# Optimization experiments

Hardware: AMD Instinct MI355X
Metric: run time of the kernel (lower is better)

Reference implementation:

```python
import jax, jax.numpy as jnp
import numpy as np
import math

COEFF_SHIFT_ARRAY = [0, 63, 31, 21, 15, 12, 10, 9, 7, 7, 6, 5, 5, 4, 4, 4, 3, 3, 3, 3, 3, 3, 2, 2, 2, 2, 2, 2, 2, 2, 2, 2, 1, 1, 1, 1, 1, 1, 1, 1, 1, 1, 1, 1, 1, 1, 1, 1, 1, 1, 1, 1, 1, 1, 1, 1, 1, 1, 1, 1, 1, 1, 1, 1]

MAX_VAL = 1023.0          # (1 << 10) - 1
QSTEP = 25.5
DEAD_ZONE_OFFSET = 85.0 / 512.0


def make_orthonormal_dct2_matrix(n):
    x = np.arange(n, dtype=np.float64).reshape(1, n)
    k = np.arange(n, dtype=np.float64).reshape(n, 1)
    mat = np.cos(math.pi / n * (x + 0.5) * k)
    mat[0, :] *= math.sqrt(1.0 / n)
    mat[1:, :] *= math.sqrt(2.0 / n)
    return jnp.asarray(mat, dtype=jnp.float32)


def setup_inputs() -> dict:
    key = jax.random.key(0)
    residual_norm = jax.random.normal(key, (256, 64, 32, 32), dtype=jnp.float32) * 0.1
    dct_mat = make_orthonormal_dct2_matrix(32)           # [32, 32], Ch == Cw
    coeff_shift = jnp.asarray(COEFF_SHIFT_ARRAY, dtype=jnp.float32)  # [64]
    return {"residual_norm": residual_norm, "dct_mat": dct_mat, "coeff_shift": coeff_shift}


def reference(residual_norm, dct_mat, coeff_shift):
    C = dct_mat
    # scale to integer-like domain
    x = residual_norm * MAX_VAL                                   # [B,Ch,H,W]
    # DCT2: coeff = C @ x @ C.T
    tmp = jnp.einsum('kh,bchw->bckw', C, x)
    coeff = jnp.einsum('lw,bckw->bckl', C, tmp)
    # dead-zone quantize with STE
    sgn = jnp.sign(coeff)
    q_abs_real = jnp.abs(coeff) / QSTEP + DEAD_ZONE_OFFSET
    q_hat = jnp.floor(q_abs_real) * sgn
    q_real = q_abs_real * sgn
    qcoeff = q_real + jax.lax.stop_gradient(q_hat - q_real)      # STE
    # dequantize with qAbs<64 interpolation correction + STE
    q_abs = jnp.abs(qcoeff)
    q_sgn = jnp.where(qcoeff < 0.0, -1.0, 1.0)
    coeff_abs = q_abs * QSTEP
    idx = jnp.clip(jax.lax.stop_gradient(q_abs).astype(jnp.int32), 0, 63)
    cs = coeff_shift[idx]
    coeff_abs2 = (q_abs + 1.0) * QSTEP
    coeff_abs_corr = ((1024.0 - cs) * coeff_abs + cs * coeff_abs2) / 1024.0
    coeff_abs_hat = jnp.where(q_abs < 64.0, coeff_abs_corr, coeff_abs)
    coeff_hat_det = coeff_abs_hat * q_sgn
    coeff_real = coeff_abs * q_sgn
    coeff_hat = coeff_real + jax.lax.stop_gradient(coeff_hat_det - coeff_real)  # STE
    # IDCT2: x = C.T @ coeff @ C
    tmp2 = jnp.einsum('hk,bckw->bchw', C, coeff_hat)
    rec = jnp.einsum('wl,bchw->bchl', C, tmp2)
    return rec / MAX_VAL
```

## Files before the change

kernel.cpp:

```cpp
#include <hip/hip_runtime.h>

typedef float f32x4 __attribute__((ext_vector_type(4)));
typedef short s16x8 __attribute__((ext_vector_type(8)));

#define QSTEP 25.5f
#define DZ (85.0f/512.0f)

__device__ __forceinline__ unsigned rne_bf16(float x) {
  unsigned u = __float_as_uint(x);
  return (u + 0x7FFFu + ((u >> 16) & 1u)) >> 16;
}

__global__ __launch_bounds__(256, 4) void vvc_mfma2_kernel(
    const float* __restrict__ resid,
    const float* __restrict__ dct,
    const float* __restrict__ cshift,
    float* __restrict__ out)
{
  __shared__ float shm[64 + 4 * 1152];
  float* Dq   = shm;
  float* Pall = shm + 64;

  const int tid  = threadIdx.x;
  const int wave = tid >> 6;
  const int lane = tid & 63;
  const int col  = lane & 15;
  const int quad = lane >> 4;
  const int k0   = quad * 8;

  unsigned short* Chi  = (unsigned short*)Pall;
  unsigned short* Clo  = Chi + 1280;
  unsigned short* CThi = Chi + 2560;
  {
    float4 cv = ((const float4*)dct)[tid];
    int k = tid >> 3, h = (tid & 7) * 4;
    float vals[4] = {cv.x, cv.y, cv.z, cv.w};
#pragma unroll
    for (int i = 0; i < 4; ++i) {
      unsigned hi = rne_bf16(vals[i]);
      float r = vals[i] - __uint_as_float(hi << 16);
      unsigned lo = rne_bf16(r);
      Chi[k * 40 + h + i]        = (unsigned short)hi;
      Clo[k * 40 + h + i]        = (unsigned short)lo;
      CThi[(h + i) * 40 + k]     = (unsigned short)hi;
    }
    if (tid < 64)
      Dq[tid] = QSTEP * ((float)tid + cshift[tid] * (1.0f / 1024.0f));
  }
  __syncthreads();

  s16x8 aChi[2], aClo[2], bCThi[2];
#pragma unroll
  for (int i = 0; i < 2; ++i) {
    aChi[i]  = *(const s16x8*)(Chi  + (16 * i + col) * 40 + k0);
    aClo[i]  = *(const s16x8*)(Clo  + (16 * i + col) * 40 + k0);
    bCThi[i] = *(const s16x8*)(CThi + (16 * i + col) * 40 + k0);
  }
  __syncthreads();

  float* Pw = Pall + wave * 1152;
  const int tile = blockIdx.x * 4 + wave;
  const float* gx = resid + (size_t)tile * 1024;
  float* gout     = out   + (size_t)tile * 1024;

  s16x8 bXhi[2], bXlo[2];
#pragma unroll
  for (int nj = 0; nj < 2; ++nj) {
#pragma unroll
    for (int j = 0; j < 8; ++j) {
      float x = gx[(k0 + j) * 32 + nj * 16 + col] * 1023.0f;
      unsigned u  = __float_as_uint(x);
      float r = x - __uint_as_float(u & 0xFFFF0000u);
      bXhi[nj][j] = (short)(u >> 16);
      bXlo[nj][j] = (short)(__float_as_uint(r) >> 16);
    }
  }

  f32x4 acc[2][2];

#pragma unroll
  for (int mi = 0; mi < 2; ++mi)
#pragma unroll
    for (int nj = 0; nj < 2; ++nj) acc[mi][nj] = (f32x4)0.0f;
#pragma unroll
  for (int mi = 0; mi < 2; ++mi)
#pragma unroll
    for (int nj = 0; nj < 2; ++nj) {
      acc[mi][nj] = __builtin_amdgcn_mfma_f32_16x16x32_bf16(aChi[mi], bXhi[nj], acc[mi][nj], 0, 0, 0);
      acc[mi][nj] = __builtin_amdgcn_mfma_f32_16x16x32_bf16(aClo[mi], bXhi[nj], acc[mi][nj], 0, 0, 0);
      acc[mi][nj] = __builtin_amdgcn_mfma_f32_16x16x32_bf16(aChi[mi], bXlo[nj], acc[mi][nj], 0, 0, 0);
    }

  unsigned* T = (unsigned*)Pw;
#pragma unroll
  for (int mi = 0; mi < 2; ++mi)
#pragma unroll
    for (int nj = 0; nj < 2; ++nj)
#pragma unroll
      for (int r = 0; r < 4; ++r) {
        float v = acc[mi][nj][r];
        unsigned u = __float_as_uint(v);
        float rr = v - __uint_as_float(u & 0xFFFF0000u);
        T[(16 * mi + 4 * quad + r) * 36 + 16 * nj + col] =
            (u >> 16) | (__float_as_uint(rr) & 0xFFFF0000u);
      }

  s16x8 tHi[2], tLo[2];
#pragma unroll
  for (int mi = 0; mi < 2; ++mi) {
    const unsigned* row = T + (16 * mi + col) * 36 + k0;
    uint4 u0 = *(const uint4*)row, u1 = *(const uint4*)(row + 4);
    s16x8 h, l;
    h[0]=(short)u0.x; h[1]=(short)u0.y; h[2]=(short)u0.z; h[3]=(short)u0.w;
    h[4]=(short)u1.x; h[5]=(short)u1.y; h[6]=(short)u1.z; h[7]=(short)u1.w;
    l[0]=(short)(u0.x>>16); l[1]=(short)(u0.y>>16); l[2]=(short)(u0.z>>16); l[3]=(short)(u0.w>>16);
    l[4]=(short)(u1.x>>16); l[5]=(short)(u1.y>>16); l[6]=(short)(u1.z>>16); l[7]=(short)(u1.w>>16);
    tHi[mi] = h; tLo[mi] = l;
  }
#pragma unroll
  for (int mi = 0; mi < 2; ++mi)
#pragma unroll
    for (int nj = 0; nj < 2; ++nj) acc[mi][nj] = (f32x4)0.0f;
#pragma unroll
  for (int mi = 0; mi < 2; ++mi)
#pragma unroll
    for (int nj = 0; nj < 2; ++nj) {
      acc[mi][nj] = __builtin_amdgcn_mfma_f32_16x16x32_bf16(tHi[mi], aChi[nj], acc[mi][nj], 0, 0, 0);
      acc[mi][nj] = __builtin_amdgcn_mfma_f32_16x16x32_bf16(tLo[mi], aChi[nj], acc[mi][nj], 0, 0, 0);
      acc[mi][nj] = __builtin_amdgcn_mfma_f32_16x16x32_bf16(tHi[mi], aClo[nj], acc[mi][nj], 0, 0, 0);
    }

  unsigned short* WT = (unsigned short*)Pw;
#pragma unroll
  for (int mi = 0; mi < 2; ++mi)
#pragma unroll
    for (int nj = 0; nj < 2; ++nj) {
      unsigned w16[4];
#pragma unroll
      for (int r = 0; r < 4; ++r) {
        float cc  = acc[mi][nj][r];
        float qa  = floorf(fabsf(cc) * (1.0f / QSTEP) + DZ);
        int   qi  = (int)qa; qi = qi > 63 ? 63 : qi;
        float lut = Dq[qi];
        float cah = (qa < 64.0f) ? lut : qa * QSTEP;
        float wv  = (cc < 0.0f) ? -cah : cah;
        w16[r] = rne_bf16(wv);
      }
      uint2 pk; pk.x = w16[0] | (w16[1] << 16); pk.y = w16[2] | (w16[3] << 16);
      *(uint2*)(WT + (16 * nj + col) * 40 + 16 * mi + 4 * quad) = pk;
    }

  s16x8 wA[2];
#pragma unroll
  for (int mi = 0; mi < 2; ++mi)
    wA[mi] = *(const s16x8*)(WT + (16 * mi + col) * 40 + k0);
#pragma unroll
  for (int mi = 0; mi < 2; ++mi)
#pragma unroll
    for (int nj = 0; nj < 2; ++nj) acc[mi][nj] = (f32x4)0.0f;
#pragma unroll
  for (int mi = 0; mi < 2; ++mi)
#pragma unroll
    for (int nj = 0; nj < 2; ++nj)
      acc[mi][nj] = __builtin_amdgcn_mfma_f32_16x16x32_bf16(wA[mi], aChi[nj], acc[mi][nj], 0, 0, 0);

  unsigned short* U = WT;
#pragma unroll
  for (int mi = 0; mi < 2; ++mi)
#pragma unroll
    for (int nj = 0; nj < 2; ++nj) {
      unsigned u16v[4];
#pragma unroll
      for (int r = 0; r < 4; ++r) u16v[r] = rne_bf16(acc[mi][nj][r]);
      uint2 pk; pk.x = u16v[0] | (u16v[1] << 16); pk.y = u16v[2] | (u16v[3] << 16);
      *(uint2*)(U + (16 * nj + col) * 40 + 16 * mi + 4 * quad) = pk;
    }

  s16x8 uA[2];
#pragma unroll
  for (int mi = 0; mi < 2; ++mi)
    uA[mi] = *(const s16x8*)(U + (16 * mi + col) * 40 + k0);
#pragma unroll
  for (int mi = 0; mi < 2; ++mi)
#pragma unroll
    for (int nj = 0; nj < 2; ++nj) acc[mi][nj] = (f32x4)0.0f;
#pragma unroll
  for (int mi = 0; mi < 2; ++mi)
#pragma unroll
    for (int nj = 0; nj < 2; ++nj)
      acc[mi][nj] = __builtin_amdgcn_mfma_f32_16x16x32_bf16(uA[mi], bCThi[nj], acc[mi][nj], 0, 0, 0);

#pragma unroll
  for (int mi = 0; mi < 2; ++mi)
#pragma unroll
    for (int nj = 0; nj < 2; ++nj)
#pragma unroll
      for (int r = 0; r < 4; ++r)
        gout[(16 * mi + 4 * quad + r) * 32 + 16 * nj + col] =
            acc[mi][nj][r] * (1.0f / 1023.0f);
}

extern "C" void kernel_launch(void* const* d_in, const int* in_sizes, int n_in,
                              void* d_out, int out_size, void* d_ws, size_t ws_size,
                              hipStream_t stream) {
  const float* resid  = (const float*)d_in[0];
  const float* dct    = (const float*)d_in[1];
  const float* cshift = (const float*)d_in[2];
  float* out = (float*)d_out;

  int tiles  = out_size / 1024;
  int blocks = tiles / 4;
  vvc_mfma2_kernel<<<blocks, 256, 0, stream>>>(resid, dct, cshift, out);
}
```

Before: 116.6 us.

## Use persistent blocks looping over tiles with register prefetch of next tile

The kernel now launches a fixed grid of 1024 blocks. Each wave loops over several 32x32 tiles, strided by 4096 tiles, and prefetches the next tile's input into registers while it computes the current one. This amortizes the per-block DCT matrix setup and bf16 splitting, and overlaps global loads with the MFMA work. The risks are higher register pressure, fewer resident waves to hide latency, and the assumption that the tile count is a multiple of 4096.

```diff
diff --git a/kernel.cpp b/kernel.cpp
--- a/kernel.cpp
+++ b/kernel.cpp
@@ -15,7 +15,8 @@
     const float* __restrict__ resid,
     const float* __restrict__ dct,
     const float* __restrict__ cshift,
-    float* __restrict__ out)
+    float* __restrict__ out,
+    int niter)
 {
   __shared__ float shm[64 + 4 * 1152];
   float* Dq   = shm;
@@ -59,145 +60,171 @@
   __syncthreads();
 
   float* Pw = Pall + wave * 1152;
-  const int tile = blockIdx.x * 4 + wave;
-  const float* gx = resid + (size_t)tile * 1024;
-  float* gout     = out   + (size_t)tile * 1024;
-
-  s16x8 bXhi[2], bXlo[2];
-#pragma unroll
-  for (int nj = 0; nj < 2; ++nj) {
-#pragma unroll
-    for (int j = 0; j < 8; ++j) {
-      float x = gx[(k0 + j) * 32 + nj * 16 + col] * 1023.0f;
-      unsigned u  = __float_as_uint(x);
-      float r = x - __uint_as_float(u & 0xFFFF0000u);
-      bXhi[nj][j] = (short)(u >> 16);
-      bXlo[nj][j] = (short)(__float_as_uint(r) >> 16);
+  const int wgid = blockIdx.x * 4 + wave;
+  const int xoff = k0 * 32 + col;
+  const float* gx = resid + (size_t)wgid * 1024 + xoff;
+  float* gout     = out   + (size_t)wgid * 1024;
+  const size_t tstride = (size_t)4096 * 1024;
+
+  float rawA[2][8], rawB[2][8];
+#pragma unroll
+  for (int nj = 0; nj < 2; ++nj)
+#pragma unroll
+    for (int j = 0; j < 8; ++j)
+      rawA[nj][j] = gx[j * 32 + nj * 16];
+
+  for (int it = 0; it < niter; ++it) {
+    if (it + 1 < niter) {
+      const float* gn = gx + (size_t)(it + 1) * tstride;
+#pragma unroll
+      for (int nj = 0; nj < 2; ++nj)
+#pragma unroll
+        for (int j = 0; j < 8; ++j)
+          rawB[nj][j] = gn[j * 32 + nj * 16];
     }
+
+    s16x8 bXhi[2], bXlo[2];
+#pragma unroll
+    for (int nj = 0; nj < 2; ++nj)
+#pragma unroll
+      for (int j = 0; j < 8; ++j) {
+        float x = rawA[nj][j] * 1023.0f;
+        unsigned u = __float_as_uint(x);
+        float r = x - __uint_as_float(u & 0xFFFF0000u);
+        bXhi[nj][j] = (short)(u >> 16);
+        bXlo[nj][j] = (short)(__float_as_uint(r) >> 16);
+      }
+
+    f32x4 acc[2][2];
+
+#pragma unroll
+    for (int mi = 0; mi < 2; ++mi)
+#pragma unroll
+      for (int nj = 0; nj < 2; ++nj) acc[mi][nj] = (f32x4)0.0f;
+#pragma unroll
+    for (int mi = 0; mi < 2; ++mi)
+#pragma unroll
+      for (int nj = 0; nj < 2; ++nj) {
+        acc[mi][nj] = __builtin_amdgcn_mfma_f32_16x16x32_bf16(aChi[mi], bXhi[nj], acc[mi][nj], 0, 0, 0);
+        acc[mi][nj] = __builtin_amdgcn_mfma_f32_16x16x32_bf16(aClo[mi], bXhi[nj], acc[mi][nj], 0, 0, 0);
+        acc[mi][nj] = __builtin_amdgcn_mfma_f32_16x16x32_bf16(aChi[mi], bXlo[nj], acc[mi][nj], 0, 0, 0);
+      }
+
+    unsigned* T = (unsigned*)Pw;
+#pragma unroll
+    for (int mi = 0; mi < 2; ++mi)
+#pragma unroll
+      for (int nj = 0; nj < 2; ++nj)
+#pragma unroll
+        for (int r = 0; r < 4; ++r) {
+          float v = acc[mi][nj][r];
+          unsigned u = __float_as_uint(v);
+          float rr = v - __uint_as_float(u & 0xFFFF0000u);
+          T[(16 * mi + 4 * quad + r) * 36 + 16 * nj + col] =
+              (u >> 16) | (__float_as_uint(rr) & 0xFFFF0000u);
+        }
+
+    s16x8 tHi[2], tLo[2];
+#pragma unroll
+    for (int mi = 0; mi < 2; ++mi) {
+      const unsigned* row = T + (16 * mi + col) * 36 + k0;
+      uint4 u0 = *(const uint4*)row, u1 = *(const uint4*)(row + 4);
+      s16x8 h, l;
+      h[0]=(short)u0.x; h[1]=(short)u0.y; h[2]=(short)u0.z; h[3]=(short)u0.w;
+      h[4]=(short)u1.x; h[5]=(short)u1.y; h[6]=(short)u1.z; h[7]=(short)u1.w;
+      l[0]=(short)(u0.x>>16); l[1]=(short)(u0.y>>16); l[2]=(short)(u0.z>>16); l[3]=(short)(u0.w>>16);
+      l[4]=(short)(u1.x>>16); l[5]=(short)(u1.y>>16); l[6]=(short)(u1.z>>16); l[7]=(short)(u1.w>>16);
+      tHi[mi] = h; tLo[mi] = l;
+    }
+#pragma unroll
+    for (int mi = 0; mi < 2; ++mi)
+#pragma unroll
+      for (int nj = 0; nj < 2; ++nj) acc[mi][nj] = (f32x4)0.0f;
+#pragma unroll
+    for (int mi = 0; mi < 2; ++mi)
+#pragma unroll
+      for (int nj = 0; nj < 2; ++nj) {
+        acc[mi][nj] = __builtin_amdgcn_mfma_f32_16x16x32_bf16(tHi[mi], aChi[nj], acc[mi][nj], 0, 0, 0);
+        acc[mi][nj] = __builtin_amdgcn_mfma_f32_16x16x32_bf16(tLo[mi], aChi[nj], acc[mi][nj], 0, 0, 0);
+        acc[mi][nj] = __builtin_amdgcn_mfma_f32_16x16x32_bf16(tHi[mi], aClo[nj], acc[mi][nj], 0, 0, 0);
+      }
+
+    unsigned short* WT = (unsigned short*)Pw;
+#pragma unroll
+    for (int mi = 0; mi < 2; ++mi)
+#pragma unroll
+      for (int nj = 0; nj < 2; ++nj) {
+        unsigned w16[4];
+#pragma unroll
+        for (int r = 0; r < 4; ++r) {
+          float cc  = acc[mi][nj][r];
+          float qa  = floorf(fabsf(cc) * (1.0f / QSTEP) + DZ);
+          int   qi  = (int)qa; qi = qi > 63 ? 63 : qi;
+          float lut = Dq[qi];
+          float cah = (qa < 64.0f) ? lut : qa * QSTEP;
+          float wv  = (cc < 0.0f) ? -cah : cah;
+          w16[r] = rne_bf16(wv);
+        }
+        uint2 pk; pk.x = w16[0] | (w16[1] << 16); pk.y = w16[2] | (w16[3] << 16);
+        *(uint2*)(WT + (16 * nj + col) * 40 + 16 * mi + 4 * quad) = pk;
+      }
+
+    s16x8 wA[2];
+#pragma unroll
+    for (int mi = 0; mi < 2; ++mi)
+      wA[mi] = *(const s16x8*)(WT + (16 * mi + col) * 40 + k0);
+#pragma unroll
+    for (int mi = 0; mi < 2; ++mi)
+#pragma unroll
+      for (int nj = 0; nj < 2; ++nj) acc[mi][nj] = (f32x4)0.0f;
+#pragma unroll
+    for (int mi = 0; mi < 2; ++mi)
+#pragma unroll
+      for (int nj = 0; nj < 2; ++nj)
+        acc[mi][nj] = __builtin_amdgcn_mfma_f32_16x16x32_bf16(wA[mi], aChi[nj], acc[mi][nj], 0, 0, 0);
+
+    unsigned short* U = WT;
+#pragma unroll
+    for (int mi = 0; mi < 2; ++mi)
+#pragma unroll
+      for (int nj = 0; nj < 2; ++nj) {
+        unsigned u16v[4];
+#pragma unroll
+        for (int r = 0; r < 4; ++r) u16v[r] = rne_bf16(acc[mi][nj][r]);
+        uint2 pk; pk.x = u16v[0] | (u16v[1] << 16); pk.y = u16v[2] | (u16v[3] << 16);
+        *(uint2*)(U + (16 * nj + col) * 40 + 16 * mi + 4 * quad) = pk;
+      }
+
+    s16x8 uA[2];
+#pragma unroll
+    for (int mi = 0; mi < 2; ++mi)
+      uA[mi] = *(const s16x8*)(U + (16 * mi + col) * 40 + k0);
+#pragma unroll
+    for (int mi = 0; mi < 2; ++mi)
+#pragma unroll
+      for (int nj = 0; nj < 2; ++nj) acc[mi][nj] = (f32x4)0.0f;
+#pragma unroll
+    for (int mi = 0; mi < 2; ++mi)
+#pragma unroll
+      for (int nj = 0; nj < 2; ++nj)
+        acc[mi][nj] = __builtin_amdgcn_mfma_f32_16x16x32_bf16(uA[mi], bCThi[nj], acc[mi][nj], 0, 0, 0);
+
+    float* go = gout + (size_t)it * tstride;
+#pragma unroll
+    for (int mi = 0; mi < 2; ++mi)
+#pragma unroll
+      for (int nj = 0; nj < 2; ++nj)
+#pragma unroll
+        for (int r = 0; r < 4; ++r)
+          go[(16 * mi + 4 * quad + r) * 32 + 16 * nj + col] =
+              acc[mi][nj][r] * (1.0f / 1023.0f);
+
+#pragma unroll
+    for (int nj = 0; nj < 2; ++nj)
+#pragma unroll
+      for (int j = 0; j < 8; ++j)
+        rawA[nj][j] = rawB[nj][j];
   }
-
-  f32x4 acc[2][2];
-
-#pragma unroll
-  for (int mi = 0; mi < 2; ++mi)
-#pragma unroll
-    for (int nj = 0; nj < 2; ++nj) acc[mi][nj] = (f32x4)0.0f;
-#pragma unroll
-  for (int mi = 0; mi < 2; ++mi)
-#pragma unroll
-    for (int nj = 0; nj < 2; ++nj) {
-      acc[mi][nj] = __builtin_amdgcn_mfma_f32_16x16x32_bf16(aChi[mi], bXhi[nj], acc[mi][nj], 0, 0, 0);
-      acc[mi][nj] = __builtin_amdgcn_mfma_f32_16x16x32_bf16(aClo[mi], bXhi[nj], acc[mi][nj], 0, 0, 0);
-      acc[mi][nj] = __builtin_amdgcn_mfma_f32_16x16x32_bf16(aChi[mi], bXlo[nj], acc[mi][nj], 0, 0, 0);
-    }
-
-  unsigned* T = (unsigned*)Pw;
-#pragma unroll
-  for (int mi = 0; mi < 2; ++mi)
-#pragma unroll
-    for (int nj = 0; nj < 2; ++nj)
-#pragma unroll
-      for (int r = 0; r < 4; ++r) {
-        float v = acc[mi][nj][r];
-        unsigned u = __float_as_uint(v);
-        float rr = v - __uint_as_float(u & 0xFFFF0000u);
-        T[(16 * mi + 4 * quad + r) * 36 + 16 * nj + col] =
-            (u >> 16) | (__float_as_uint(rr) & 0xFFFF0000u);
-      }
-
-  s16x8 tHi[2], tLo[2];
-#pragma unroll
-  for (int mi = 0; mi < 2; ++mi) {
-    const unsigned* row = T + (16 * mi + col) * 36 + k0;
-    uint4 u0 = *(const uint4*)row, u1 = *(const uint4*)(row + 4);
-    s16x8 h, l;
-    h[0]=(short)u0.x; h[1]=(short)u0.y; h[2]=(short)u0.z; h[3]=(short)u0.w;
-    h[4]=(short)u1.x; h[5]=(short)u1.y; h[6]=(short)u1.z; h[7]=(short)u1.w;
-    l[0]=(short)(u0.x>>16); l[1]=(short)(u0.y>>16); l[2]=(short)(u0.z>>16); l[3]=(short)(u0.w>>16);
-    l[4]=(short)(u1.x>>16); l[5]=(short)(u1.y>>16); l[6]=(short)(u1.z>>16); l[7]=(short)(u1.w>>16);
-    tHi[mi] = h; tLo[mi] = l;
-  }
-#pragma unroll
-  for (int mi = 0; mi < 2; ++mi)
-#pragma unroll
-    for (int nj = 0; nj < 2; ++nj) acc[mi][nj] = (f32x4)0.0f;
-#pragma unroll
-  for (int mi = 0; mi < 2; ++mi)
-#pragma unroll
-    for (int nj = 0; nj < 2; ++nj) {
-      acc[mi][nj] = __builtin_amdgcn_mfma_f32_16x16x32_bf16(tHi[mi], aChi[nj], acc[mi][nj], 0, 0, 0);
-      acc[mi][nj] = __builtin_amdgcn_mfma_f32_16x16x32_bf16(tLo[mi], aChi[nj], acc[mi][nj], 0, 0, 0);
-      acc[mi][nj] = __builtin_amdgcn_mfma_f32_16x16x32_bf16(tHi[mi], aClo[nj], acc[mi][nj], 0, 0, 0);
-    }
-
-  unsigned short* WT = (unsigned short*)Pw;
-#pragma unroll
-  for (int mi = 0; mi < 2; ++mi)
-#pragma unroll
-    for (int nj = 0; nj < 2; ++nj) {
-      unsigned w16[4];
-#pragma unroll
-      for (int r = 0; r < 4; ++r) {
-        float cc  = acc[mi][nj][r];
-        float qa  = floorf(fabsf(cc) * (1.0f / QSTEP) + DZ);
-        int   qi  = (int)qa; qi = qi > 63 ? 63 : qi;
-        float lut = Dq[qi];
-        float cah = (qa < 64.0f) ? lut : qa * QSTEP;
-        float wv  = (cc < 0.0f) ? -cah : cah;
-        w16[r] = rne_bf16(wv);
-      }
-      uint2 pk; pk.x = w16[0] | (w16[1] << 16); pk.y = w16[2] | (w16[3] << 16);
-      *(uint2*)(WT + (16 * nj + col) * 40 + 16 * mi + 4 * quad) = pk;
-    }
-
-  s16x8 wA[2];
-#pragma unroll
-  for (int mi = 0; mi < 2; ++mi)
-    wA[mi] = *(const s16x8*)(WT + (16 * mi + col) * 40 + k0);
-#pragma unroll
-  for (int mi = 0; mi < 2; ++mi)
-#pragma unroll
-    for (int nj = 0; nj < 2; ++nj) acc[mi][nj] = (f32x4)0.0f;
-#pragma unroll
-  for (int mi = 0; mi < 2; ++mi)
-#pragma unroll
-    for (int nj = 0; nj < 2; ++nj)
-      acc[mi][nj] = __builtin_amdgcn_mfma_f32_16x16x32_bf16(wA[mi], aChi[nj], acc[mi][nj], 0, 0, 0);
-
-  unsigned short* U = WT;
-#pragma unroll
-  for (int mi = 0; mi < 2; ++mi)
-#pragma unroll
-    for (int nj = 0; nj < 2; ++nj) {
-      unsigned u16v[4];
-#pragma unroll
-      for (int r = 0; r < 4; ++r) u16v[r] = rne_bf16(acc[mi][nj][r]);
-      uint2 pk; pk.x = u16v[0] | (u16v[1] << 16); pk.y = u16v[2] | (u16v[3] << 16);
-      *(uint2*)(U + (16 * nj + col) * 40 + 16 * mi + 4 * quad) = pk;
-    }
-
-  s16x8 uA[2];
-#pragma unroll
-  for (int mi = 0; mi < 2; ++mi)
-    uA[mi] = *(const s16x8*)(U + (16 * mi + col) * 40 + k0);
-#pragma unroll
-  for (int mi = 0; mi < 2; ++mi)
-#pragma unroll
-    for (int nj = 0; nj < 2; ++nj) acc[mi][nj] = (f32x4)0.0f;
-#pragma unroll
-  for (int mi = 0; mi < 2; ++mi)
-#pragma unroll
-    for (int nj = 0; nj < 2; ++nj)
-      acc[mi][nj] = __builtin_amdgcn_mfma_f32_16x16x32_bf16(uA[mi], bCThi[nj], acc[mi][nj], 0, 0, 0);
-
-#pragma unroll
-  for (int mi = 0; mi < 2; ++mi)
-#pragma unroll
-    for (int nj = 0; nj < 2; ++nj)
-#pragma unroll
-      for (int r = 0; r < 4; ++r)
-        gout[(16 * mi + 4 * quad + r) * 32 + 16 * nj + col] =
-            acc[mi][nj][r] * (1.0f / 1023.0f);
 }
 
 extern "C" void kernel_launch(void* const* d_in, const int* in_sizes, int n_in,
@@ -209,6 +236,7 @@
   float* out = (float*)d_out;
 
   int tiles  = out_size / 1024;
-  int blocks = tiles / 4;
-  vvc_mfma2_kernel<<<blocks, 256, 0, stream>>>(resid, dct, cshift, out);
+  int blocks = 1024;
+  int niter  = tiles / 4096;
+  vvc_mfma2_kernel<<<blocks, 256, 0, stream>>>(resid, dct, cshift, out, niter);
 }
```

After: 116.1 us. About the same (-0.4%).
